# Kernel optimization log

Hardware: AMD Instinct MI355X
Metric: run time of the kernel (lower is better)

Reference implementation:

```python
import jax, jax.numpy as jnp
import numpy as np

T = 8192          # total prefill tokens (single sequence, cu_seqlens=[0,T])
H = 16            # local num heads (k == v heads)
D = 128           # head_k_dim == head_v_dim
K = 4             # causal conv kernel width
CHUNK = 64        # chunk size used by chunk_kda
EPS = 1e-6


def setup_inputs() -> dict:
    key = jax.random.key(0)
    ks = jax.random.split(key, 6)
    return {
        "mixed_qkv": jax.random.normal(ks[0], (T, 3 * H * D), dtype=jnp.float32),
        "forget_gate": jax.random.normal(ks[1], (T, H * D), dtype=jnp.float32),
        "beta": jax.random.normal(ks[2], (T, H), dtype=jnp.float32),
        "conv_weights": jax.random.normal(ks[3], (3 * H * D, K), dtype=jnp.float32) * 0.1,
        "dt_bias": jax.random.normal(ks[4], (H, D), dtype=jnp.float32),
        "alog": jax.random.normal(ks[5], (H,), dtype=jnp.float32),
    }


def _l2norm(x):
    return x * jax.lax.rsqrt(jnp.sum(x * x, axis=-1, keepdims=True) + EPS)


def _causal_conv1d(x, w):
    # x: [T, C], w: [C, K] depthwise causal conv + SiLU (causal_conv1d_fn)
    xpad = jnp.pad(x, ((K - 1, 0), (0, 0)))
    out = sum(xpad[j:j + T] * w[:, j] for j in range(K))
    return jax.nn.silu(out)


def _kda_forward(mixed_qkv, forget_gate, beta, conv_weights, dt_bias, alog):
    x = _causal_conv1d(mixed_qkv, conv_weights)               # [T, 3*H*D]
    q, k, v = jnp.split(x, [H * D, 2 * H * D], axis=-1)
    q = _l2norm(q.reshape(T, H, D)) * (D ** -0.5)             # scale = head_k_dim^-0.5
    k = _l2norm(k.reshape(T, H, D))
    v = v.reshape(T, H, D)
    # fused_kda_gate: g = -exp(A_log) * softplus(g_raw + dt_bias), per (head, dim)
    g = -jnp.exp(alog)[None, :, None] * jax.nn.softplus(
        forget_gate.reshape(T, H, D) + dt_bias[None])
    decay = jnp.exp(g)                                        # [T, H, D]
    b = jax.nn.sigmoid(beta)                                  # [T, H]

    def step(S, inp):
        # S: [H, Dk, Dv]
        q_t, k_t, v_t, d_t, b_t = inp
        S = S * d_t[:, :, None]                               # per-dim forget gate on key dim
        kmem = jnp.einsum('hk,hkv->hv', k_t, S)
        delta = b_t[:, None] * (v_t - kmem)                   # beta-scaled delta rule
        S = S + jnp.einsum('hk,hv->hkv', k_t, delta)
        o_t = jnp.einsum('hk,hkv->hv', q_t, S)
        return S, o_t

    @jax.checkpoint
    def chunk_fn(S, ch):
        return jax.lax.scan(step, S, ch)

    NC = T // CHUNK
    chunked = lambda a: a.reshape(NC, CHUNK, H, D)
    S0 = jnp.zeros((H, D, D), dtype=jnp.float32)
    _, o = jax.lax.scan(chunk_fn, S0,
                        (chunked(q), chunked(k), chunked(v), chunked(decay),
                         b.reshape(NC, CHUNK, H)))
    return o.reshape(T, H, D)


def reference(mixed_qkv, forget_gate, beta, conv_weights, dt_bias, alog):
    return _kda_forward(mixed_qkv, forget_gate, beta, conv_weights, dt_bias, alog)
```

## Files before the change

kernel.cpp:

```cpp
#include <hip/hip_runtime.h>
#include <math.h>

#define NH 16
#define HD 128
#define CH1 2048
#define CH3 6144
#define CK 64
#define NC 128
#define PCH 132
#define MP 68

#define QT_OFF  0u
#define KBT_OFF 16777216u
#define U0_OFF  33554432u
#define Z_OFF   50331648u
#define W_OFF   67108864u
#define ECG_OFF 75497472u
#define SLAB_OFF 75759616u

__global__ __launch_bounds__(512, 2)
void kda_chunk(const float* __restrict__ mixed, const float* __restrict__ fg,
               const float* __restrict__ beta, const float* __restrict__ cw,
               const float* __restrict__ dtb, const float* __restrict__ alog,
               float* __restrict__ qt_g, float* __restrict__ kbt_g,
               float* __restrict__ u0_g, float* __restrict__ z_g,
               float* __restrict__ w_g, float* __restrict__ ecg_g) {
  __shared__ float lds[35520];
  float* kL  = lds;
  float* qL  = lds + 8448;
  float* cgL = lds + 16896;
  float* ML  = lds + 25344;
  float* NT  = lds + 29696;
  float* GB  = lds + 34048;
  float* bL  = lds + 34816;
  float* nrm = lds + 34880;

  const int tid = threadIdx.x;
  const int bid = blockIdx.x;
  const int c = bid >> 4, h = bid & 15;
  const int t0 = c * CK;
  const float ea = __expf(alog[h]);

  {
    size_t wb = (size_t)bid * 4096;
#pragma unroll
    for (int i = 0; i < 8; ++i) w_g[wb + tid + 512 * i] = 0.f;
  }

  for (int it = 0; it < 16; ++it) {
    int cell = tid + (it << 9);
    int d = cell & 127, t = cell >> 7;
    float x = fg[(size_t)(t0 + t) * CH1 + h * HD + d] + dtb[h * HD + d];
    float sp = (x > 20.f) ? x : log1pf(__expf(x));
    cgL[t * PCH + d] = -ea * sp;
  }
  if (tid < 64) bL[tid] = 1.f / (1.f + __expf(-beta[(size_t)(t0 + tid) * NH + h]));
  __syncthreads();

  if (tid < 128) {
    float a = 0.f;
    for (int t = 0; t < 64; ++t) { a += cgL[t * PCH + tid]; cgL[t * PCH + tid] = a; }
    ecg_g[(size_t)bid * 128 + tid] = __expf(a);
  }

  for (int it = 0; it < 32; ++it) {
    int cell = tid + (it << 9);
    int d = cell & 127, sec = (cell >> 7) & 1, t = cell >> 8;
    int ch = sec * CH1 + h * HD + d;
    float4 w4 = ((const float4*)cw)[ch];
    int rbase = t0 + t - 3;
    float acc;
    if (rbase >= 0) {
      const float* mp = mixed + (size_t)rbase * CH3 + ch;
      acc = mp[0] * w4.x + mp[CH3] * w4.y + mp[2 * CH3] * w4.z + mp[3 * CH3] * w4.w;
    } else {
      acc = 0.f;
      if (rbase + 0 >= 0) acc += mixed[(size_t)(rbase + 0) * CH3 + ch] * w4.x;
      if (rbase + 1 >= 0) acc += mixed[(size_t)(rbase + 1) * CH3 + ch] * w4.y;
      if (rbase + 2 >= 0) acc += mixed[(size_t)(rbase + 2) * CH3 + ch] * w4.z;
      acc += mixed[(size_t)(rbase + 3) * CH3 + ch] * w4.w;
    }
    acc = acc / (1.f + __expf(-acc));
    float* dst = (sec == 0) ? qL : kL;
    dst[t * PCH + d] = acc;
  }
  __syncthreads();

  {
    int sec = tid >> 8, t = (tid >> 2) & 63, r = tid & 3;
    const float* src = (sec == 0) ? qL : kL;
    float s = 0.f;
#pragma unroll
    for (int i = 0; i < 8; ++i) {
      float4 v = *(const float4*)(src + t * PCH + r * 32 + i * 4);
      s += v.x * v.x + v.y * v.y + v.z * v.z + v.w * v.w;
    }
    nrm[tid] = s;
  }
  __syncthreads();
  if (tid < 128) {
    int sec = tid >> 6, t = tid & 63;
    float s = nrm[sec * 256 + t * 4] + nrm[sec * 256 + t * 4 + 1] +
              nrm[sec * 256 + t * 4 + 2] + nrm[sec * 256 + t * 4 + 3];
    float inv = rsqrtf(s + 1e-6f);
    if (sec == 0) inv *= 0.08838834764831845f;
    nrm[512 + tid] = inv;
  }
  __syncthreads();
  for (int it = 0; it < 8; ++it) {
    int f4 = tid + (it << 9);
    int sec = f4 >> 11, t = (f4 >> 5) & 63, d4 = f4 & 31;
    float* dst = (sec == 0) ? qL : kL;
    float inv = nrm[512 + sec * 64 + t];
    float4 v = *(float4*)(dst + t * PCH + d4 * 4);
    v.x *= inv; v.y *= inv; v.z *= inv; v.w *= inv;
    *(float4*)(dst + t * PCH + d4 * 4) = v;
  }
  __syncthreads();

  {
    int tW = tid >> 3, g = tid & 7;
    size_t qb = (size_t)bid * 8192 + g * 1024 + tW * 16;
    size_t kb = (size_t)bid * 8192;
#pragma unroll
    for (int i = 0; i < 4; ++i) {
      int d = g * 16 + 4 * i;
      float4 qv = *(const float4*)(qL + tW * PCH + d);
      float4 cg4 = *(const float4*)(cgL + tW * PCH + d);
      float4 o;
      o.x = qv.x * __expf(cg4.x); o.y = qv.y * __expf(cg4.y);
      o.z = qv.z * __expf(cg4.z); o.w = qv.w * __expf(cg4.w);
      *(float4*)(qt_g + qb + 4 * i) = o;
      float4 kv = *(const float4*)(kL + tW * PCH + d);
      float4 c63 = *(const float4*)(cgL + 63 * PCH + d);
      kbt_g[kb + (size_t)(d + 0) * 64 + tW] = kv.x * __expf(c63.x - cg4.x);
      kbt_g[kb + (size_t)(d + 1) * 64 + tW] = kv.y * __expf(c63.y - cg4.y);
      kbt_g[kb + (size_t)(d + 2) * 64 + tW] = kv.z * __expf(c63.z - cg4.z);
      kbt_g[kb + (size_t)(d + 3) * 64 + tW] = kv.w * __expf(c63.w - cg4.w);
    }
  }

  int taD = 0, saD = 0;
  float accA[16], accW[16];
  if (tid < 272) {
    int L = tid >> 1, dh = tid & 1;
    int tt = (int)((sqrtf(8.f * L + 1.f) - 1.f) * 0.5f);
    while ((tt + 1) * (tt + 2) / 2 <= L) ++tt;
    while (tt * (tt + 1) / 2 > L) --tt;
    int ss = L - tt * (tt + 1) / 2;
    taD = tt * 4; saD = ss * 4;
#pragma unroll
    for (int i = 0; i < 16; ++i) { accA[i] = 0.f; accW[i] = 0.f; }
    int d0 = dh << 6;
    for (int d = d0; d < d0 + 64; d += 4) {
      float kt[4][4], qt4[4][4], ct[4][4], ks4[4][4], cs4[4][4];
#pragma unroll
      for (int i = 0; i < 4; ++i) {
        *(float4*)kt[i]  = *(const float4*)(kL + (taD + i) * PCH + d);
        *(float4*)qt4[i] = *(const float4*)(qL + (taD + i) * PCH + d);
        *(float4*)ct[i]  = *(const float4*)(cgL + (taD + i) * PCH + d);
        *(float4*)ks4[i] = *(const float4*)(kL + (saD + i) * PCH + d);
        *(float4*)cs4[i] = *(const float4*)(cgL + (saD + i) * PCH + d);
      }
#pragma unroll
      for (int i = 0; i < 4; ++i)
#pragma unroll
        for (int j = 0; j < 4; ++j)
#pragma unroll
          for (int dd = 0; dd < 4; ++dd) {
            float diff = ct[i][dd] - cs4[j][dd];
            float e = __expf(fminf(diff, 0.f));
            float m = e * ks4[j][dd];
            accA[i * 4 + j] += kt[i][dd] * m;
            accW[i * 4 + j] += qt4[i][dd] * m;
          }
    }
    if (dh) {
#pragma unroll
      for (int i = 0; i < 16; ++i) {
        NT[L * 32 + i] = accA[i];
        NT[L * 32 + 16 + i] = accW[i];
      }
    }
  }
  __syncthreads();
  if (tid < 272 && !(tid & 1)) {
    int L = tid >> 1;
#pragma unroll
    for (int i = 0; i < 16; ++i) {
      accA[i] += NT[L * 32 + i];
      accW[i] += NT[L * 32 + 16 + i];
    }
    size_t wb = (size_t)bid * 4096;
#pragma unroll
    for (int i = 0; i < 4; ++i)
#pragma unroll
      for (int j = 0; j < 4; ++j) {
        int t = taD + i, s = saD + j;
        if (s < t) ML[t * MP + s] = bL[t] * accA[i * 4 + j];
        float wv = (s <= t) ? accW[i * 4 + j] : 0.f;
        w_g[wb + (size_t)(s >> 3) * 512 + t * 8 + (s & 7)] = wv;
      }
  }
  __syncthreads();

  for (int i = tid; i < 4352; i += 512) NT[i] = 0.f;
  __syncthreads();
  if (tid < 64) {
    int b4 = tid >> 4, j = tid & 15, bo = b4 * 16;
    NT[(bo + j) * MP + bo + j] = 1.f;
    for (int t = j + 1; t < 16; ++t) {
      float s = 0.f;
      for (int sx = j; sx < t; ++sx)
        s += ML[(bo + t) * MP + bo + sx] * NT[(bo + j) * MP + bo + sx];
      NT[(bo + j) * MP + bo + t] = -s;
    }
  }
  __syncthreads();
  for (int lev = 1; lev <= 3; ++lev) {
    int nb = 4 - lev;
    for (int idx = tid; idx < nb * 256; idx += 512) {
      int J = idx >> 8, I = J + lev;
      int i = (idx >> 4) & 15, j = idx & 15;
      float s = 0.f;
      for (int P = J; P < I; ++P)
#pragma unroll 4
        for (int p = 0; p < 16; ++p)
          s += ML[(16 * I + i) * MP + 16 * P + p] * NT[(16 * J + j) * MP + 16 * P + p];
      GB[J * 256 + i * 16 + j] = s;
    }
    __syncthreads();
    for (int idx = tid; idx < nb * 256; idx += 512) {
      int J = idx >> 8, I = J + lev;
      int i = (idx >> 4) & 15, j = idx & 15;
      float s = 0.f;
#pragma unroll 4
      for (int p = 0; p < 16; ++p)
        s += NT[(16 * I + p) * MP + 16 * I + i] * GB[J * 256 + p * 16 + j];
      NT[(16 * J + j) * MP + 16 * I + i] = -s;
    }
    __syncthreads();
  }

  {
    int tW = tid >> 3, g = tid & 7;
    float b = bL[tW];
#pragma unroll
    for (int i = 0; i < 4; ++i) {
      int d = g * 16 + 4 * i;
      float4 kv = *(const float4*)(kL + tW * PCH + d);
      float4 cg4 = *(const float4*)(cgL + tW * PCH + d);
      float4 r;
      r.x = b * kv.x * __expf(cg4.x); r.y = b * kv.y * __expf(cg4.y);
      r.z = b * kv.z * __expf(cg4.z); r.w = b * kv.w * __expf(cg4.w);
      *(float4*)(qL + tW * PCH + d) = r;
    }
  }
  __syncthreads();
  {
    int t4 = tid >> 5, c4 = tid & 31;
    float acc[4][4];
#pragma unroll
    for (int i = 0; i < 4; ++i)
#pragma unroll
      for (int j = 0; j < 4; ++j) acc[i][j] = 0.f;
    for (int s = 0; s < 64; ++s) {
      float nv[4], rv[4];
      *(float4*)nv = *(const float4*)(NT + s * MP + t4 * 4);
      *(float4*)rv = *(const float4*)(qL + s * PCH + c4 * 4);
#pragma unroll
      for (int i = 0; i < 4; ++i)
#pragma unroll
        for (int j = 0; j < 4; ++j) acc[i][j] += nv[i] * rv[j];
    }
    size_t zb = (size_t)bid * 8192 + (size_t)(c4 >> 2) * 1024 + (c4 & 3) * 4;
#pragma unroll
    for (int i = 0; i < 4; ++i) {
      float4 o; o.x = acc[i][0]; o.y = acc[i][1]; o.z = acc[i][2]; o.w = acc[i][3];
      *(float4*)(z_g + zb + (size_t)(t4 * 4 + i) * 16) = o;
    }
  }
  __syncthreads();

  for (int it = 0; it < 16; ++it) {
    int cell = tid + (it << 9);
    int d = cell & 127, t = cell >> 7;
    int ch = 2 * CH1 + h * HD + d;
    float4 w4 = ((const float4*)cw)[ch];
    int rbase = t0 + t - 3;
    float acc;
    if (rbase >= 0) {
      const float* mp = mixed + (size_t)rbase * CH3 + ch;
      acc = mp[0] * w4.x + mp[CH3] * w4.y + mp[2 * CH3] * w4.z + mp[3 * CH3] * w4.w;
    } else {
      acc = 0.f;
      if (rbase + 0 >= 0) acc += mixed[(size_t)(rbase + 0) * CH3 + ch] * w4.x;
      if (rbase + 1 >= 0) acc += mixed[(size_t)(rbase + 1) * CH3 + ch] * w4.y;
      if (rbase + 2 >= 0) acc += mixed[(size_t)(rbase + 2) * CH3 + ch] * w4.z;
      acc += mixed[(size_t)(rbase + 3) * CH3 + ch] * w4.w;
    }
    acc = acc / (1.f + __expf(-acc));
    qL[t * PCH + d] = bL[t] * acc;
  }
  __syncthreads();
  {
    int t4 = tid >> 5, c4 = tid & 31;
    float acc[4][4];
#pragma unroll
    for (int i = 0; i < 4; ++i)
#pragma unroll
      for (int j = 0; j < 4; ++j) acc[i][j] = 0.f;
    for (int s = 0; s < 64; ++s) {
      float nv[4], rv[4];
      *(float4*)nv = *(const float4*)(NT + s * MP + t4 * 4);
      *(float4*)rv = *(const float4*)(qL + s * PCH + c4 * 4);
#pragma unroll
      for (int i = 0; i < 4; ++i)
#pragma unroll
        for (int j = 0; j < 4; ++j) acc[i][j] += nv[i] * rv[j];
    }
#pragma unroll
    for (int i = 0; i < 4; ++i) {
      size_t ob = ((size_t)(t0 + t4 * 4 + i) * NH + h) * HD + c4 * 4;
      float4 o; o.x = acc[i][0]; o.y = acc[i][1]; o.z = acc[i][2]; o.w = acc[i][3];
      *(float4*)(u0_g + ob) = o;
    }
  }
}

#define PT 68
#define PG 544

__global__ __launch_bounds__(512, 2)
void kda_scan3(const float* __restrict__ qt_g, const float* __restrict__ kbt_g,
               const float* __restrict__ u0_g, const float* __restrict__ z_g,
               const float* __restrict__ w_g, const float* __restrict__ ecg_g,
               float* __restrict__ out, float* __restrict__ slabs) {
  __shared__ float Tp[4352], Op[4352];
  __shared__ float Wp[2176];
  __shared__ float Sl[1536];
  __shared__ float Un[512];
  __shared__ float Ut[544];
  (void)slabs;
  const int tid = threadIdx.x;
  const int bid = blockIdx.x;
  const int h = bid & 15, vg = bid >> 4;
  const int gA = tid >> 6, tA = tid & 63;
  const int tH = (tid & 255) >> 2;
  const int jH = (tid & 3) << 1;
  const int kC = tid & 127;
  const int jq = ((tid >> 7) & 1) << 2;
  const int gB = (tid >> 6) & 3;

  for (int i = tid; i < 1536; i += 512) Sl[i] = 0.f;
  __syncthreads();

  float OsA = 0.f, OsB = 0.f;

  for (int c = 0; c < NC; ++c) {
    const int ch = c * 16 + h;
    float z[16], q[16];
    {
      const float* zb = z_g + (size_t)ch * 8192 + gA * 1024 + tA * 16;
      const float* qb = qt_g + (size_t)ch * 8192 + gA * 1024 + tA * 16;
#pragma unroll
      for (int i = 0; i < 4; ++i) {
        *(float4*)(z + 4 * i) = *(const float4*)(zb + 4 * i);
        *(float4*)(q + 4 * i) = *(const float4*)(qb + 4 * i);
      }
    }
    float w16[16];
    float u0a = 0.f, u0b = 0.f;
    float kv[64], eC = 0.f;
    if (tid < 256) {
      const float* kb = kbt_g + (size_t)ch * 8192 + (size_t)kC * 64;
#pragma unroll
      for (int t4 = 0; t4 < 16; ++t4)
        *(float4*)(kv + 4 * t4) = *(const float4*)(kb + 4 * t4);
      eC = ecg_g[(size_t)ch * 128 + kC];
      const float* ub = u0_g + ((size_t)(c * 64 + tH) * NH + h) * HD + vg * 8 + jH;
      u0a = ub[0]; u0b = ub[1];
    } else {
      const float* wb = w_g + (size_t)ch * 4096 + (size_t)(gB * 2) * 512 + tA * 8;
      *(float4*)w16       = *(const float4*)(wb);
      *(float4*)(w16 + 4) = *(const float4*)(wb + 4);
      *(float4*)(w16 + 8)  = *(const float4*)(wb + 512);
      *(float4*)(w16 + 12) = *(const float4*)(wb + 516);
    }

    if (tid >= 256 && c > 0) {
      float O2a = 0.f, O2b = 0.f;
#pragma unroll
      for (int g = 0; g < 4; ++g) {
        O2a += Wp[g * PG + jH * PT + tH];
        O2b += Wp[g * PG + (jH + 1) * PT + tH];
      }
      float* ob = out + ((size_t)((c - 1) * 64 + tH) * NH + h) * HD + vg * 8 + jH;
      ob[0] = OsA + O2a; ob[1] = OsB + O2b;
    }
    {
      float Ta[8], Oa[8];
#pragma unroll
      for (int j = 0; j < 8; ++j) { Ta[j] = 0.f; Oa[j] = 0.f; }
#pragma unroll
      for (int dd = 0; dd < 16; ++dd) {
        float s8[8];
        const float* sr = Sl + (gA * 16 + dd) * 12;
        *(float4*)s8 = *(const float4*)(sr);
        *(float4*)(s8 + 4) = *(const float4*)(sr + 4);
        float zz = z[dd], qq = q[dd];
#pragma unroll
        for (int j = 0; j < 8; ++j) { Ta[j] += zz * s8[j]; Oa[j] += qq * s8[j]; }
      }
#pragma unroll
      for (int j = 0; j < 8; ++j) {
        Tp[gA * PG + j * PT + tA] = Ta[j];
        Op[gA * PG + j * PT + tA] = Oa[j];
      }
    }
    __syncthreads();

    if (tid < 256) {
      float Tsa = 0.f, Tsb = 0.f;
#pragma unroll
      for (int g = 0; g < 8; ++g) {
        Tsa += Tp[g * PG + jH * PT + tH];
        Tsb += Tp[g * PG + (jH + 1) * PT + tH];
      }
      float Ua = u0a - Tsa, Ub = u0b - Tsb;
      Un[tH * 8 + jH] = Ua; Un[tH * 8 + jH + 1] = Ub;
      Ut[jH * PT + tH] = Ua; Ut[(jH + 1) * PT + tH] = Ub;
    } else {
      float Os1 = 0.f, Os2 = 0.f;
#pragma unroll
      for (int g = 0; g < 8; ++g) {
        Os1 += Op[g * PG + jH * PT + tH];
        Os2 += Op[g * PG + (jH + 1) * PT + tH];
      }
      OsA = Os1; OsB = Os2;
    }
    __syncthreads();

    if (tid < 256) {
      float a0 = 0.f, a1 = 0.f, a2 = 0.f, a3 = 0.f;
      const float* u0r = Ut + (jq + 0) * PT;
      const float* u1r = Ut + (jq + 1) * PT;
      const float* u2r = Ut + (jq + 2) * PT;
      const float* u3r = Ut + (jq + 3) * PT;
#pragma unroll
      for (int t4 = 0; t4 < 16; ++t4) {
        float k0 = kv[4 * t4], k1 = kv[4 * t4 + 1], k2 = kv[4 * t4 + 2], k3 = kv[4 * t4 + 3];
        float4 ua = *(const float4*)(u0r + 4 * t4);
        float4 ub = *(const float4*)(u1r + 4 * t4);
        float4 uc = *(const float4*)(u2r + 4 * t4);
        float4 ud = *(const float4*)(u3r + 4 * t4);
        a0 += k0 * ua.x + k1 * ua.y + k2 * ua.z + k3 * ua.w;
        a1 += k0 * ub.x + k1 * ub.y + k2 * ub.z + k3 * ub.w;
        a2 += k0 * uc.x + k1 * uc.y + k2 * uc.z + k3 * uc.w;
        a3 += k0 * ud.x + k1 * ud.y + k2 * ud.z + k3 * ud.w;
      }
      float* sp = Sl + kC * 12 + jq;
      float4 s = *(float4*)sp;
      s.x = eC * s.x + a0; s.y = eC * s.y + a1;
      s.z = eC * s.z + a2; s.w = eC * s.w + a3;
      *(float4*)sp = s;
    } else {
      float Wa[8];
#pragma unroll
      for (int j = 0; j < 8; ++j) Wa[j] = 0.f;
#pragma unroll
      for (int sp = 0; sp < 16; ++sp) {
        const float* ur = Un + (gB * 16 + sp) * 8;
        float u8[8];
        *(float4*)u8 = *(const float4*)(ur);
        *(float4*)(u8 + 4) = *(const float4*)(ur + 4);
        float wv = w16[sp];
#pragma unroll
        for (int j = 0; j < 8; ++j) Wa[j] += wv * u8[j];
      }
#pragma unroll
      for (int j = 0; j < 8; ++j) Wp[gB * PG + j * PT + tA] = Wa[j];
    }
    __syncthreads();
  }

  if (tid >= 256) {
    float O2a = 0.f, O2b = 0.f;
#pragma unroll
    for (int g = 0; g < 4; ++g) {
      O2a += Wp[g * PG + jH * PT + tH];
      O2b += Wp[g * PG + (jH + 1) * PT + tH];
    }
    float* ob = out + ((size_t)((NC - 1) * 64 + tH) * NH + h) * HD + vg * 8 + jH;
    ob[0] = OsA + O2a; ob[1] = OsB + O2b;
  }
}

extern "C" void kernel_launch(void* const* d_in, const int* in_sizes, int n_in,
                              void* d_out, int out_size, void* d_ws, size_t ws_size,
                              hipStream_t stream) {
  const float* mixed = (const float*)d_in[0];
  const float* fg    = (const float*)d_in[1];
  const float* beta  = (const float*)d_in[2];
  const float* cw    = (const float*)d_in[3];
  const float* dtb   = (const float*)d_in[4];
  const float* alog  = (const float*)d_in[5];
  float* ws = (float*)d_ws;
  float* qt_g  = ws + QT_OFF;
  float* kbt_g = ws + KBT_OFF;
  float* u0_g  = ws + U0_OFF;
  float* z_g   = ws + Z_OFF;
  float* w_g   = ws + W_OFF;
  float* ecg_g = ws + ECG_OFF;
  float* slabs = ws + SLAB_OFF;

  hipLaunchKernelGGL(kda_chunk, dim3(NC * NH), dim3(512), 0, stream,
                     mixed, fg, beta, cw, dtb, alog,
                     qt_g, kbt_g, u0_g, z_g, w_g, ecg_g);
  hipLaunchKernelGGL(kda_scan3, dim3(256), dim3(512), 0, stream,
                     qt_g, kbt_g, u0_g, z_g, w_g, ecg_g, (float*)d_out, slabs);
  (void)in_sizes; (void)n_in; (void)out_size; (void)ws_size;
}
```

Before: 1.847 ms.

## Double kda_chunk block size to 1024 threads and split triangular work four ways

Raises the kda_chunk block from 512 to 1024 threads and re-partitions every phase (gate, conv, norm, output writes, the two 64x128 matmuls) so each thread does half the work. The triangular A/W tile computation is now split four ways over the head dimension, with the partial sums combined by warp shuffles instead of an LDS round-trip and an extra barrier. It also rotates the d offset per thread to spread LDS bank accesses. The aim is more parallelism per chunk; the risk is register pressure under launch_bounds(1024,4) and reduced occupancy because of the larger LDS footprint.

```diff
diff --git a/kernel.cpp b/kernel.cpp
--- a/kernel.cpp
+++ b/kernel.cpp
@@ -18,14 +18,14 @@
 #define ECG_OFF 75497472u
 #define SLAB_OFF 75759616u
 
-__global__ __launch_bounds__(512, 2)
+__global__ __launch_bounds__(1024, 4)
 void kda_chunk(const float* __restrict__ mixed, const float* __restrict__ fg,
                const float* __restrict__ beta, const float* __restrict__ cw,
                const float* __restrict__ dtb, const float* __restrict__ alog,
                float* __restrict__ qt_g, float* __restrict__ kbt_g,
                float* __restrict__ u0_g, float* __restrict__ z_g,
                float* __restrict__ w_g, float* __restrict__ ecg_g) {
-  __shared__ float lds[35520];
+  __shared__ float lds[36032];
   float* kL  = lds;
   float* qL  = lds + 8448;
   float* cgL = lds + 16896;
@@ -44,11 +44,11 @@
   {
     size_t wb = (size_t)bid * 4096;
 #pragma unroll
-    for (int i = 0; i < 8; ++i) w_g[wb + tid + 512 * i] = 0.f;
-  }
-
-  for (int it = 0; it < 16; ++it) {
-    int cell = tid + (it << 9);
+    for (int i = 0; i < 4; ++i) w_g[wb + tid + 1024 * i] = 0.f;
+  }
+
+  for (int it = 0; it < 8; ++it) {
+    int cell = tid + (it << 10);
     int d = cell & 127, t = cell >> 7;
     float x = fg[(size_t)(t0 + t) * CH1 + h * HD + d] + dtb[h * HD + d];
     float sp = (x > 20.f) ? x : log1pf(__expf(x));
@@ -63,8 +63,8 @@
     ecg_g[(size_t)bid * 128 + tid] = __expf(a);
   }
 
-  for (int it = 0; it < 32; ++it) {
-    int cell = tid + (it << 9);
+  for (int it = 0; it < 16; ++it) {
+    int cell = tid + (it << 10);
     int d = cell & 127, sec = (cell >> 7) & 1, t = cell >> 8;
     int ch = sec * CH1 + h * HD + d;
     float4 w4 = ((const float4*)cw)[ch];
@@ -87,12 +87,12 @@
   __syncthreads();
 
   {
-    int sec = tid >> 8, t = (tid >> 2) & 63, r = tid & 3;
+    int sec = tid >> 9, t = (tid >> 3) & 63, r = tid & 7;
     const float* src = (sec == 0) ? qL : kL;
     float s = 0.f;
 #pragma unroll
-    for (int i = 0; i < 8; ++i) {
-      float4 v = *(const float4*)(src + t * PCH + r * 32 + i * 4);
+    for (int i = 0; i < 4; ++i) {
+      float4 v = *(const float4*)(src + t * PCH + r * 16 + i * 4);
       s += v.x * v.x + v.y * v.y + v.z * v.z + v.w * v.w;
     }
     nrm[tid] = s;
@@ -100,18 +100,19 @@
   __syncthreads();
   if (tid < 128) {
     int sec = tid >> 6, t = tid & 63;
-    float s = nrm[sec * 256 + t * 4] + nrm[sec * 256 + t * 4 + 1] +
-              nrm[sec * 256 + t * 4 + 2] + nrm[sec * 256 + t * 4 + 3];
+    float s = 0.f;
+#pragma unroll
+    for (int r = 0; r < 8; ++r) s += nrm[sec * 512 + t * 8 + r];
     float inv = rsqrtf(s + 1e-6f);
     if (sec == 0) inv *= 0.08838834764831845f;
-    nrm[512 + tid] = inv;
-  }
-  __syncthreads();
-  for (int it = 0; it < 8; ++it) {
-    int f4 = tid + (it << 9);
+    nrm[1024 + tid] = inv;
+  }
+  __syncthreads();
+  for (int it = 0; it < 4; ++it) {
+    int f4 = tid + (it << 10);
     int sec = f4 >> 11, t = (f4 >> 5) & 63, d4 = f4 & 31;
     float* dst = (sec == 0) ? qL : kL;
-    float inv = nrm[512 + sec * 64 + t];
+    float inv = nrm[1024 + sec * 64 + t];
     float4 v = *(float4*)(dst + t * PCH + d4 * 4);
     v.x *= inv; v.y *= inv; v.z *= inv; v.w *= inv;
     *(float4*)(dst + t * PCH + d4 * 4) = v;
@@ -119,12 +120,12 @@
   __syncthreads();
 
   {
-    int tW = tid >> 3, g = tid & 7;
-    size_t qb = (size_t)bid * 8192 + g * 1024 + tW * 16;
+    int tW = tid >> 4, g = tid & 15;
+    size_t qb = (size_t)bid * 8192 + (size_t)(g >> 1) * 1024 + tW * 16 + (g & 1) * 8;
     size_t kb = (size_t)bid * 8192;
 #pragma unroll
-    for (int i = 0; i < 4; ++i) {
-      int d = g * 16 + 4 * i;
+    for (int i = 0; i < 2; ++i) {
+      int d = g * 8 + 4 * i;
       float4 qv = *(const float4*)(qL + tW * PCH + d);
       float4 cg4 = *(const float4*)(cgL + tW * PCH + d);
       float4 o;
@@ -140,71 +141,65 @@
     }
   }
 
-  int taD = 0, saD = 0;
-  float accA[16], accW[16];
-  if (tid < 272) {
-    int L = tid >> 1, dh = tid & 1;
+  if (tid < 544) {
+    int L = tid >> 2, dh = tid & 3;
     int tt = (int)((sqrtf(8.f * L + 1.f) - 1.f) * 0.5f);
     while ((tt + 1) * (tt + 2) / 2 <= L) ++tt;
     while (tt * (tt + 1) / 2 > L) --tt;
     int ss = L - tt * (tt + 1) / 2;
-    taD = tt * 4; saD = ss * 4;
+    int taD = tt * 4, saD = ss * 4;
+    float accA[16], accW[16];
 #pragma unroll
     for (int i = 0; i < 16; ++i) { accA[i] = 0.f; accW[i] = 0.f; }
-    int d0 = dh << 6;
-    for (int d = d0; d < d0 + 64; d += 4) {
-      float kt[4][4], qt4[4][4], ct[4][4], ks4[4][4], cs4[4][4];
+    for (int s4 = 0; s4 < 8; ++s4) {
+      int d = (dh << 5) + (((s4 + L + (dh << 1)) & 7) << 2);
+      float ks4v[4][4], cs4v[4][4];
+#pragma unroll
+      for (int j = 0; j < 4; ++j) {
+        *(float4*)ks4v[j] = *(const float4*)(kL + (saD + j) * PCH + d);
+        *(float4*)cs4v[j] = *(const float4*)(cgL + (saD + j) * PCH + d);
+      }
 #pragma unroll
       for (int i = 0; i < 4; ++i) {
-        *(float4*)kt[i]  = *(const float4*)(kL + (taD + i) * PCH + d);
-        *(float4*)qt4[i] = *(const float4*)(qL + (taD + i) * PCH + d);
-        *(float4*)ct[i]  = *(const float4*)(cgL + (taD + i) * PCH + d);
-        *(float4*)ks4[i] = *(const float4*)(kL + (saD + i) * PCH + d);
-        *(float4*)cs4[i] = *(const float4*)(cgL + (saD + i) * PCH + d);
-      }
+        float kt4[4], qt4[4], ct4[4];
+        *(float4*)kt4 = *(const float4*)(kL + (taD + i) * PCH + d);
+        *(float4*)qt4 = *(const float4*)(qL + (taD + i) * PCH + d);
+        *(float4*)ct4 = *(const float4*)(cgL + (taD + i) * PCH + d);
+#pragma unroll
+        for (int j = 0; j < 4; ++j)
+#pragma unroll
+          for (int dd = 0; dd < 4; ++dd) {
+            float diff = ct4[dd] - cs4v[j][dd];
+            float e = __expf(fminf(diff, 0.f));
+            float m = e * ks4v[j][dd];
+            accA[i * 4 + j] += kt4[dd] * m;
+            accW[i * 4 + j] += qt4[dd] * m;
+          }
+      }
+    }
+#pragma unroll
+    for (int i = 0; i < 16; ++i) {
+      accA[i] += __shfl_xor(accA[i], 1);
+      accA[i] += __shfl_xor(accA[i], 2);
+      accW[i] += __shfl_xor(accW[i], 1);
+      accW[i] += __shfl_xor(accW[i], 2);
+    }
+    if (dh == 0) {
+      size_t wb = (size_t)bid * 4096;
 #pragma unroll
       for (int i = 0; i < 4; ++i)
 #pragma unroll
-        for (int j = 0; j < 4; ++j)
-#pragma unroll
-          for (int dd = 0; dd < 4; ++dd) {
-            float diff = ct[i][dd] - cs4[j][dd];
-            float e = __expf(fminf(diff, 0.f));
-            float m = e * ks4[j][dd];
-            accA[i * 4 + j] += kt[i][dd] * m;
-            accW[i * 4 + j] += qt4[i][dd] * m;
-          }
-    }
-    if (dh) {
-#pragma unroll
-      for (int i = 0; i < 16; ++i) {
-        NT[L * 32 + i] = accA[i];
-        NT[L * 32 + 16 + i] = accW[i];
-      }
-    }
-  }
-  __syncthreads();
-  if (tid < 272 && !(tid & 1)) {
-    int L = tid >> 1;
-#pragma unroll
-    for (int i = 0; i < 16; ++i) {
-      accA[i] += NT[L * 32 + i];
-      accW[i] += NT[L * 32 + 16 + i];
-    }
-    size_t wb = (size_t)bid * 4096;
-#pragma unroll
-    for (int i = 0; i < 4; ++i)
-#pragma unroll
-      for (int j = 0; j < 4; ++j) {
-        int t = taD + i, s = saD + j;
-        if (s < t) ML[t * MP + s] = bL[t] * accA[i * 4 + j];
-        float wv = (s <= t) ? accW[i * 4 + j] : 0.f;
-        w_g[wb + (size_t)(s >> 3) * 512 + t * 8 + (s & 7)] = wv;
-      }
-  }
-  __syncthreads();
-
-  for (int i = tid; i < 4352; i += 512) NT[i] = 0.f;
+        for (int j = 0; j < 4; ++j) {
+          int t = taD + i, s = saD + j;
+          if (s < t) ML[t * MP + s] = bL[t] * accA[i * 4 + j];
+          float wv = (s <= t) ? accW[i * 4 + j] : 0.f;
+          w_g[wb + (size_t)(s >> 3) * 512 + t * 8 + (s & 7)] = wv;
+        }
+    }
+  }
+  __syncthreads();
+
+  for (int i = tid; i < 4352; i += 1024) NT[i] = 0.f;
   __syncthreads();
   if (tid < 64) {
     int b4 = tid >> 4, j = tid & 15, bo = b4 * 16;
@@ -219,7 +214,7 @@
   __syncthreads();
   for (int lev = 1; lev <= 3; ++lev) {
     int nb = 4 - lev;
-    for (int idx = tid; idx < nb * 256; idx += 512) {
+    for (int idx = tid; idx < nb * 256; idx += 1024) {
       int J = idx >> 8, I = J + lev;
       int i = (idx >> 4) & 15, j = idx & 15;
       float s = 0.f;
@@ -230,7 +225,7 @@
       GB[J * 256 + i * 16 + j] = s;
     }
     __syncthreads();
-    for (int idx = tid; idx < nb * 256; idx += 512) {
+    for (int idx = tid; idx < nb * 256; idx += 1024) {
       int J = idx >> 8, I = J + lev;
       int i = (idx >> 4) & 15, j = idx & 15;
       float s = 0.f;
@@ -243,11 +238,11 @@
   }
 
   {
-    int tW = tid >> 3, g = tid & 7;
+    int tW = tid >> 4, g = tid & 15;
     float b = bL[tW];
 #pragma unroll
-    for (int i = 0; i < 4; ++i) {
-      int d = g * 16 + 4 * i;
+    for (int i = 0; i < 2; ++i) {
+      int d = g * 8 + 4 * i;
       float4 kv = *(const float4*)(kL + tW * PCH + d);
       float4 cg4 = *(const float4*)(cgL + tW * PCH + d);
       float4 r;
@@ -258,32 +253,33 @@
   }
   __syncthreads();
   {
-    int t4 = tid >> 5, c4 = tid & 31;
-    float acc[4][4];
-#pragma unroll
-    for (int i = 0; i < 4; ++i)
+    int t2 = tid >> 5, c4 = tid & 31;
+    float acc[2][4];
+#pragma unroll
+    for (int i = 0; i < 2; ++i)
 #pragma unroll
       for (int j = 0; j < 4; ++j) acc[i][j] = 0.f;
     for (int s = 0; s < 64; ++s) {
-      float nv[4], rv[4];
-      *(float4*)nv = *(const float4*)(NT + s * MP + t4 * 4);
+      float2 nv = *(const float2*)(NT + s * MP + t2 * 2);
+      float rv[4];
       *(float4*)rv = *(const float4*)(qL + s * PCH + c4 * 4);
 #pragma unroll
-      for (int i = 0; i < 4; ++i)
-#pragma unroll
-        for (int j = 0; j < 4; ++j) acc[i][j] += nv[i] * rv[j];
+      for (int j = 0; j < 4; ++j) {
+        acc[0][j] += nv.x * rv[j];
+        acc[1][j] += nv.y * rv[j];
+      }
     }
     size_t zb = (size_t)bid * 8192 + (size_t)(c4 >> 2) * 1024 + (c4 & 3) * 4;
 #pragma unroll
-    for (int i = 0; i < 4; ++i) {
+    for (int i = 0; i < 2; ++i) {
       float4 o; o.x = acc[i][0]; o.y = acc[i][1]; o.z = acc[i][2]; o.w = acc[i][3];
-      *(float4*)(z_g + zb + (size_t)(t4 * 4 + i) * 16) = o;
-    }
-  }
-  __syncthreads();
-
-  for (int it = 0; it < 16; ++it) {
-    int cell = tid + (it << 9);
+      *(float4*)(z_g + zb + (size_t)(t2 * 2 + i) * 16) = o;
+    }
+  }
+  __syncthreads();
+
+  for (int it = 0; it < 8; ++it) {
+    int cell = tid + (it << 10);
     int d = cell & 127, t = cell >> 7;
     int ch = 2 * CH1 + h * HD + d;
     float4 w4 = ((const float4*)cw)[ch];
@@ -304,24 +300,25 @@
   }
   __syncthreads();
   {
-    int t4 = tid >> 5, c4 = tid & 31;
-    float acc[4][4];
-#pragma unroll
-    for (int i = 0; i < 4; ++i)
+    int t2 = tid >> 5, c4 = tid & 31;
+    float acc[2][4];
+#pragma unroll
+    for (int i = 0; i < 2; ++i)
 #pragma unroll
       for (int j = 0; j < 4; ++j) acc[i][j] = 0.f;
     for (int s = 0; s < 64; ++s) {
-      float nv[4], rv[4];
-      *(float4*)nv = *(const float4*)(NT + s * MP + t4 * 4);
+      float2 nv = *(const float2*)(NT + s * MP + t2 * 2);
+      float rv[4];
       *(float4*)rv = *(const float4*)(qL + s * PCH + c4 * 4);
 #pragma unroll
-      for (int i = 0; i < 4; ++i)
-#pragma unroll
-        for (int j = 0; j < 4; ++j) acc[i][j] += nv[i] * rv[j];
-    }
-#pragma unroll
-    for (int i = 0; i < 4; ++i) {
-      size_t ob = ((size_t)(t0 + t4 * 4 + i) * NH + h) * HD + c4 * 4;
+      for (int j = 0; j < 4; ++j) {
+        acc[0][j] += nv.x * rv[j];
+        acc[1][j] += nv.y * rv[j];
+      }
+    }
+#pragma unroll
+    for (int i = 0; i < 2; ++i) {
+      size_t ob = ((size_t)(t0 + t2 * 2 + i) * NH + h) * HD + c4 * 4;
       float4 o; o.x = acc[i][0]; o.y = acc[i][1]; o.z = acc[i][2]; o.w = acc[i][3];
       *(float4*)(u0_g + ob) = o;
     }
@@ -514,7 +511,7 @@
   float* ecg_g = ws + ECG_OFF;
   float* slabs = ws + SLAB_OFF;
 
-  hipLaunchKernelGGL(kda_chunk, dim3(NC * NH), dim3(512), 0, stream,
+  hipLaunchKernelGGL(kda_chunk, dim3(NC * NH), dim3(1024), 0, stream,
                      mixed, fg, beta, cw, dtb, alog,
                      qt_g, kbt_g, u0_g, z_g, w_g, ecg_g);
   hipLaunchKernelGGL(kda_scan3, dim3(256), dim3(512), 0, stream,
```

Result: faster. 1.621 ms (-12.2%).
